# Optimization experiments

Hardware: AMD Instinct MI355X
Metric: run time of the kernel (lower is better)

Reference implementation:

```python
import jax, jax.numpy as jnp
import numpy as np

N_SRC = 50000   # nodes of src type
N_TRG = 50000   # nodes of trg type
H = 256         # hidden_size
E = 300000      # number of labeled edges for this message type


def setup_inputs() -> dict:
    key = jax.random.key(0)
    k0, k1, k2, k3 = jax.random.split(key, 4)
    x_src = jax.random.normal(k0, (N_SRC, H), dtype=jnp.float32)
    x_trg = jax.random.normal(k1, (N_TRG, H), dtype=jnp.float32)
    # nn.Parameter(torch.rand(H, H) * 0.01)
    R = jax.random.uniform(k2, (H, H), dtype=jnp.float32) * 0.01
    edge_index = jax.random.randint(k3, (2, E), 0, N_SRC, dtype=jnp.int64)
    return {"x_src": x_src, "x_trg": x_trg, "R": R, "edge_index": edge_index}


def reference(x_src, x_trg, R, edge_index):
    # Gather per-edge endpoint embeddings (index_select on dim 0).
    nodes_left = x_src[edge_index[0]]    # (E, H)
    nodes_right = x_trg[edge_index[1]]   # (E, H)
    # Original: sum((nodes_right @ R) @ nodes_left.T, dim=-1)
    # == (nodes_right @ R) @ nodes_left.sum(0)  -- same math, avoids the E x E
    # intermediate which is infeasible to materialize at this scale.
    left_sum = nodes_left.sum(axis=0)    # (H,)
    scores = (nodes_right @ R) @ left_sum  # (E,)
    return scores
```

## Files before the change

### kernel.cpp

```cpp
#include <hip/hip_runtime.h>

#define HDIM 256
#define CSB  1024
#define RDB  1024

__global__ void k_zero(uint4* __restrict__ p, int n4) {
    int i = blockIdx.x * blockDim.x + threadIdx.x;
    if (i < n4) p[i] = make_uint4(0u, 0u, 0u, 0u);
}

__global__ void k_count(const int4* __restrict__ src4, const int* __restrict__ src,
                        int E, unsigned int* __restrict__ cnt) {
    int i = blockIdx.x * blockDim.x + threadIdx.x;
    int E4 = E >> 2;
    if (i < E4) {
        int4 v = src4[i];
        atomicAdd(&cnt[v.x], 1u); atomicAdd(&cnt[v.y], 1u);
        atomicAdd(&cnt[v.z], 1u); atomicAdd(&cnt[v.w], 1u);
    }
    if (i < (E & 3)) atomicAdd(&cnt[src[(E4 << 2) + i]], 1u);
}

__global__ __launch_bounds__(256)
void k_colsum(const float4* __restrict__ xs4, const unsigned int* __restrict__ cnt,
              int Ns, float* __restrict__ pT) {
    const int lane = threadIdx.x & 63;
    const int wv = blockIdx.x * 4 + (threadIdx.x >> 6);
    const int NW = CSB * 4;
    float4 acc = make_float4(0.f, 0.f, 0.f, 0.f);

    float c0 = 0.f, c1 = 0.f, c2 = 0.f, c3 = 0.f;
    float4 x0 = make_float4(0,0,0,0), x1 = x0, x2 = x0, x3 = x0;
    int r = wv;
    if (r          < Ns) { c0 = (float)cnt[r];          x0 = xs4[(size_t)r * 64 + lane]; }
    if (r + NW     < Ns) { c1 = (float)cnt[r + NW];     x1 = xs4[(size_t)(r + NW) * 64 + lane]; }
    if (r + 2 * NW < Ns) { c2 = (float)cnt[r + 2 * NW]; x2 = xs4[(size_t)(r + 2 * NW) * 64 + lane]; }
    if (r + 3 * NW < Ns) { c3 = (float)cnt[r + 3 * NW]; x3 = xs4[(size_t)(r + 3 * NW) * 64 + lane]; }

    for (; r + 7 * NW < Ns; r += 4 * NW) {
        const int p = r + 4 * NW;
        float  nc0 = (float)cnt[p];           float4 nx0 = xs4[(size_t)p * 64 + lane];
        float  nc1 = (float)cnt[p + NW];      float4 nx1 = xs4[(size_t)(p + NW) * 64 + lane];
        float  nc2 = (float)cnt[p + 2 * NW];  float4 nx2 = xs4[(size_t)(p + 2 * NW) * 64 + lane];
        float  nc3 = (float)cnt[p + 3 * NW];  float4 nx3 = xs4[(size_t)(p + 3 * NW) * 64 + lane];
        acc.x += c0 * x0.x; acc.y += c0 * x0.y; acc.z += c0 * x0.z; acc.w += c0 * x0.w;
        acc.x += c1 * x1.x; acc.y += c1 * x1.y; acc.z += c1 * x1.z; acc.w += c1 * x1.w;
        acc.x += c2 * x2.x; acc.y += c2 * x2.y; acc.z += c2 * x2.z; acc.w += c2 * x2.w;
        acc.x += c3 * x3.x; acc.y += c3 * x3.y; acc.z += c3 * x3.z; acc.w += c3 * x3.w;
        c0 = nc0; x0 = nx0; c1 = nc1; x1 = nx1;
        c2 = nc2; x2 = nx2; c3 = nc3; x3 = nx3;
    }
    acc.x += c0 * x0.x; acc.y += c0 * x0.y; acc.z += c0 * x0.z; acc.w += c0 * x0.w;
    acc.x += c1 * x1.x; acc.y += c1 * x1.y; acc.z += c1 * x1.z; acc.w += c1 * x1.w;
    acc.x += c2 * x2.x; acc.y += c2 * x2.y; acc.z += c2 * x2.z; acc.w += c2 * x2.w;
    acc.x += c3 * x3.x; acc.y += c3 * x3.y; acc.z += c3 * x3.z; acc.w += c3 * x3.w;
    for (int s = r + 4 * NW; s < Ns; s += NW) {
        float  cc = (float)cnt[s];
        float4 xx = xs4[(size_t)s * 64 + lane];
        acc.x += cc * xx.x; acc.y += cc * xx.y; acc.z += cc * xx.z; acc.w += cc * xx.w;
    }

    __shared__ float s[4 * HDIM];
    const int col = lane * 4;
    const int rowOff = threadIdx.x >> 6;
    s[rowOff * HDIM + col + 0] = acc.x;
    s[rowOff * HDIM + col + 1] = acc.y;
    s[rowOff * HDIM + col + 2] = acc.z;
    s[rowOff * HDIM + col + 3] = acc.w;
    __syncthreads();
    const int tid = threadIdx.x;
    float part = (s[tid] + s[HDIM + tid]) + (s[2 * HDIM + tid] + s[3 * HDIM + tid]);
    pT[(size_t)tid * CSB + blockIdx.x] = part;
}

__global__ __launch_bounds__(256)
void k_reduceT(const float* __restrict__ pT, float* __restrict__ ls) {
    const int h = blockIdx.x;
    const int tid = threadIdx.x;
    const float* row = pT + (size_t)h * CSB;
    float a = (row[tid] + row[tid + 256]) + (row[tid + 512] + row[tid + 768]);
    #pragma unroll
    for (int o = 32; o > 0; o >>= 1) a += __shfl_down(a, o, 64);
    __shared__ float s[4];
    if ((tid & 63) == 0) s[tid >> 6] = a;
    __syncthreads();
    if (tid == 0) ls[h] = (s[0] + s[1]) + (s[2] + s[3]);
}

__global__ __launch_bounds__(256)
void k_matvec(const float* __restrict__ Rm, const float* __restrict__ ls,
              float* __restrict__ v) {
    const int i = blockIdx.x;
    const int tid = threadIdx.x;
    float a = Rm[(size_t)i * HDIM + tid] * ls[tid];
    #pragma unroll
    for (int o = 32; o > 0; o >>= 1) a += __shfl_down(a, o, 64);
    __shared__ float s[4];
    if ((tid & 63) == 0) s[tid >> 6] = a;
    __syncthreads();
    if (tid == 0) v[i] = (s[0] + s[1]) + (s[2] + s[3]);
}

__global__ __launch_bounds__(256)
void k_rowdot(const float4* __restrict__ xt4, const float* __restrict__ v,
              int N, float* __restrict__ t) {
    const int lane = threadIdx.x & 63;
    const float4 vr = ((const float4*)v)[lane];
    const int wv = blockIdx.x * 4 + (threadIdx.x >> 6);
    const int NW = RDB * 4;

    float4 x0 = make_float4(0,0,0,0), x1 = x0, x2 = x0, x3 = x0;
    int r = wv;
    if (r          < N) x0 = xt4[(size_t)r * 64 + lane];
    if (r + NW     < N) x1 = xt4[(size_t)(r + NW) * 64 + lane];
    if (r + 2 * NW < N) x2 = xt4[(size_t)(r + 2 * NW) * 64 + lane];
    if (r + 3 * NW < N) x3 = xt4[(size_t)(r + 3 * NW) * 64 + lane];

#define RD_DOT(X) ((X).x * vr.x + (X).y * vr.y + (X).z * vr.z + (X).w * vr.w)
    for (; r + 7 * NW < N; r += 4 * NW) {
        const int p = r + 4 * NW;
        float4 nx0 = xt4[(size_t)p * 64 + lane];
        float4 nx1 = xt4[(size_t)(p + NW) * 64 + lane];
        float4 nx2 = xt4[(size_t)(p + 2 * NW) * 64 + lane];
        float4 nx3 = xt4[(size_t)(p + 3 * NW) * 64 + lane];
        float d0 = RD_DOT(x0), d1 = RD_DOT(x1), d2 = RD_DOT(x2), d3 = RD_DOT(x3);
        #pragma unroll
        for (int o = 32; o > 0; o >>= 1) {
            d0 += __shfl_down(d0, o, 64); d1 += __shfl_down(d1, o, 64);
            d2 += __shfl_down(d2, o, 64); d3 += __shfl_down(d3, o, 64);
        }
        if (lane == 0) { t[r] = d0; t[r + NW] = d1; t[r + 2 * NW] = d2; t[r + 3 * NW] = d3; }
        x0 = nx0; x1 = nx1; x2 = nx2; x3 = nx3;
    }
    {
        float d0 = RD_DOT(x0), d1 = RD_DOT(x1), d2 = RD_DOT(x2), d3 = RD_DOT(x3);
        #pragma unroll
        for (int o = 32; o > 0; o >>= 1) {
            d0 += __shfl_down(d0, o, 64); d1 += __shfl_down(d1, o, 64);
            d2 += __shfl_down(d2, o, 64); d3 += __shfl_down(d3, o, 64);
        }
        if (lane == 0) {
            if (r          < N) t[r]          = d0;
            if (r + NW     < N) t[r + NW]     = d1;
            if (r + 2 * NW < N) t[r + 2 * NW] = d2;
            if (r + 3 * NW < N) t[r + 3 * NW] = d3;
        }
    }
    for (int s = r + 4 * NW; s < N; s += NW) {
        float4 xx = xt4[(size_t)s * 64 + lane];
        float d = RD_DOT(xx);
        #pragma unroll
        for (int o = 32; o > 0; o >>= 1) d += __shfl_down(d, o, 64);
        if (lane == 0) t[s] = d;
    }
#undef RD_DOT
}

__global__ void k_gather(const int4* __restrict__ trg4, const int* __restrict__ trg, int E,
                         const float* __restrict__ t,
                         float4* __restrict__ out4, float* __restrict__ out) {
    int i = blockIdx.x * blockDim.x + threadIdx.x;
    int E4 = E >> 2;
    if (i < E4) {
        int4 v = trg4[i];
        out4[i] = make_float4(t[v.x], t[v.y], t[v.z], t[v.w]);
    }
    if (i < (E & 3)) {
        int e = (E4 << 2) + i;
        out[e] = t[trg[e]];
    }
}

extern "C" void kernel_launch(void* const* d_in, const int* in_sizes, int n_in,
                              void* d_out, int out_size, void* d_ws, size_t ws_size,
                              hipStream_t stream) {
    const float* x_src = (const float*)d_in[0];
    const float* x_trg = (const float*)d_in[1];
    const float* Rm    = (const float*)d_in[2];
    const int*   edge  = (const int*)d_in[3];
    float* out = (float*)d_out;

    const int Ns = in_sizes[0] / HDIM;
    const int Nt = in_sizes[1] / HDIM;
    const int E  = in_sizes[3] / 2;

    char* ws = (char*)d_ws;
    size_t off = 0;
    auto alloc = [&](size_t bytes) -> void* {
        void* p = ws + off;
        off = (off + bytes + 255) & ~(size_t)255;
        return p;
    };
    unsigned int* cnt = (unsigned int*)alloc((size_t)Ns * sizeof(unsigned int));
    float* pT = (float*)alloc((size_t)HDIM * CSB * sizeof(float));
    float* ls = (float*)alloc(HDIM * sizeof(float));
    float* v  = (float*)alloc(HDIM * sizeof(float));
    float* t  = (float*)alloc((size_t)Nt * sizeof(float));
    (void)ws_size; (void)n_in; (void)out_size;

    const int n4 = (Ns + 3) / 4;
    k_zero<<<(n4 + 255) / 256, 256, 0, stream>>>((uint4*)cnt, n4);

    const int E4 = E >> 2;
    const int cntThreads = (E4 > 0 ? E4 : 1);
    k_count<<<(cntThreads + 255) / 256, 256, 0, stream>>>(
        (const int4*)edge, edge, E, cnt);

    k_colsum<<<CSB, 256, 0, stream>>>((const float4*)x_src, cnt, Ns, pT);

    k_reduceT<<<HDIM, 256, 0, stream>>>(pT, ls);

    k_matvec<<<HDIM, 256, 0, stream>>>(Rm, ls, v);

    k_rowdot<<<RDB, 256, 0, stream>>>((const float4*)x_trg, v, Nt, t);

    k_gather<<<(cntThreads + 255) / 256, 256, 0, stream>>>(
        (const int4*)(edge + E), edge + E, E, t, (float4*)out, out);
}
```

Baseline: 54.18 us.

## Fuse column-sum reduction into matvec and use 1024-thread colsum blocks

The column-sum kernel now runs 256 blocks of 1024 threads, reducing 16 wave partials in shared memory and writing row-major partials. The separate transpose-reduce and matvec kernels are merged into one kernel where each block redundantly sums the 256 partials before its dot product with a row of R. This removes one kernel launch and the transposed partial layout. In exchange, every matvec block re-reads the full 256x256 partial array, and the colsum runs fewer, larger blocks.

```diff
diff --git a/kernel.cpp b/kernel.cpp
--- a/kernel.cpp
+++ b/kernel.cpp
@@ -1,8 +1,10 @@
 #include <hip/hip_runtime.h>
 
 #define HDIM 256
-#define CSB  1024
+#define CSB  256
+#define CSW  (CSB * 16)
 #define RDB  1024
+#define RNW  (RDB * 4)
 
 __global__ void k_zero(uint4* __restrict__ p, int n4) {
     int i = blockIdx.x * blockDim.x + threadIdx.x;
@@ -21,12 +23,13 @@
     if (i < (E & 3)) atomicAdd(&cnt[src[(E4 << 2) + i]], 1u);
 }
 
-__global__ __launch_bounds__(256)
+__global__ __launch_bounds__(1024)
 void k_colsum(const float4* __restrict__ xs4, const unsigned int* __restrict__ cnt,
-              int Ns, float* __restrict__ pT) {
+              int Ns, float* __restrict__ P) {
     const int lane = threadIdx.x & 63;
-    const int wv = blockIdx.x * 4 + (threadIdx.x >> 6);
-    const int NW = CSB * 4;
+    const int w    = threadIdx.x >> 6;
+    const int wv   = blockIdx.x * 16 + w;
+    const int NW   = CSW;
     float4 acc = make_float4(0.f, 0.f, 0.f, 0.f);
 
     float c0 = 0.f, c1 = 0.f, c2 = 0.f, c3 = 0.f;
@@ -60,45 +63,47 @@
         acc.x += cc * xx.x; acc.y += cc * xx.y; acc.z += cc * xx.z; acc.w += cc * xx.w;
     }
 
-    __shared__ float s[4 * HDIM];
+    __shared__ float s[16 * HDIM];
     const int col = lane * 4;
-    const int rowOff = threadIdx.x >> 6;
-    s[rowOff * HDIM + col + 0] = acc.x;
-    s[rowOff * HDIM + col + 1] = acc.y;
-    s[rowOff * HDIM + col + 2] = acc.z;
-    s[rowOff * HDIM + col + 3] = acc.w;
-    __syncthreads();
+    s[w * HDIM + col + 0] = acc.x;
+    s[w * HDIM + col + 1] = acc.y;
+    s[w * HDIM + col + 2] = acc.z;
+    s[w * HDIM + col + 3] = acc.w;
+    __syncthreads();
+    {
+        const int q = threadIdx.x >> 8;
+        const int h = threadIdx.x & 255;
+        float f = (s[(q * 4 + 0) * HDIM + h] + s[(q * 4 + 1) * HDIM + h])
+                + (s[(q * 4 + 2) * HDIM + h] + s[(q * 4 + 3) * HDIM + h]);
+        __syncthreads();
+        s[(q * 4) * HDIM + h] = f;
+    }
+    __syncthreads();
+    if (threadIdx.x < HDIM) {
+        const int h = threadIdx.x;
+        P[(size_t)blockIdx.x * HDIM + h] =
+            (s[0 * HDIM + h] + s[4 * HDIM + h]) + (s[8 * HDIM + h] + s[12 * HDIM + h]);
+    }
+}
+
+__global__ __launch_bounds__(256)
+void k_mv(const float* __restrict__ P, const float* __restrict__ Rm,
+          float* __restrict__ v) {
     const int tid = threadIdx.x;
-    float part = (s[tid] + s[HDIM + tid]) + (s[2 * HDIM + tid] + s[3 * HDIM + tid]);
-    pT[(size_t)tid * CSB + blockIdx.x] = part;
-}
-
-__global__ __launch_bounds__(256)
-void k_reduceT(const float* __restrict__ pT, float* __restrict__ ls) {
-    const int h = blockIdx.x;
-    const int tid = threadIdx.x;
-    const float* row = pT + (size_t)h * CSB;
-    float a = (row[tid] + row[tid + 256]) + (row[tid + 512] + row[tid + 768]);
+    __shared__ float lss[HDIM];
+    float a = 0.f;
+    #pragma unroll 16
+    for (int b = 0; b < CSB; ++b) a += P[(size_t)b * HDIM + tid];
+    lss[tid] = a;
+    __syncthreads();
+
+    float m = Rm[(size_t)blockIdx.x * HDIM + tid] * lss[tid];
     #pragma unroll
-    for (int o = 32; o > 0; o >>= 1) a += __shfl_down(a, o, 64);
+    for (int o = 32; o > 0; o >>= 1) m += __shfl_down(m, o, 64);
     __shared__ float s[4];
-    if ((tid & 63) == 0) s[tid >> 6] = a;
-    __syncthreads();
-    if (tid == 0) ls[h] = (s[0] + s[1]) + (s[2] + s[3]);
-}
-
-__global__ __launch_bounds__(256)
-void k_matvec(const float* __restrict__ Rm, const float* __restrict__ ls,
-              float* __restrict__ v) {
-    const int i = blockIdx.x;
-    const int tid = threadIdx.x;
-    float a = Rm[(size_t)i * HDIM + tid] * ls[tid];
-    #pragma unroll
-    for (int o = 32; o > 0; o >>= 1) a += __shfl_down(a, o, 64);
-    __shared__ float s[4];
-    if ((tid & 63) == 0) s[tid >> 6] = a;
-    __syncthreads();
-    if (tid == 0) v[i] = (s[0] + s[1]) + (s[2] + s[3]);
+    if ((tid & 63) == 0) s[tid >> 6] = m;
+    __syncthreads();
+    if (tid == 0) v[blockIdx.x] = (s[0] + s[1]) + (s[2] + s[3]);
 }
 
 __global__ __launch_bounds__(256)
@@ -107,7 +112,7 @@
     const int lane = threadIdx.x & 63;
     const float4 vr = ((const float4*)v)[lane];
     const int wv = blockIdx.x * 4 + (threadIdx.x >> 6);
-    const int NW = RDB * 4;
+    const int NW = RNW;
 
     float4 x0 = make_float4(0,0,0,0), x1 = x0, x2 = x0, x3 = x0;
     int r = wv;
@@ -192,8 +197,7 @@
         return p;
     };
     unsigned int* cnt = (unsigned int*)alloc((size_t)Ns * sizeof(unsigned int));
-    float* pT = (float*)alloc((size_t)HDIM * CSB * sizeof(float));
-    float* ls = (float*)alloc(HDIM * sizeof(float));
+    float* P  = (float*)alloc((size_t)CSB * HDIM * sizeof(float));
     float* v  = (float*)alloc(HDIM * sizeof(float));
     float* t  = (float*)alloc((size_t)Nt * sizeof(float));
     (void)ws_size; (void)n_in; (void)out_size;
@@ -206,11 +210,9 @@
     k_count<<<(cntThreads + 255) / 256, 256, 0, stream>>>(
         (const int4*)edge, edge, E, cnt);
 
-    k_colsum<<<CSB, 256, 0, stream>>>((const float4*)x_src, cnt, Ns, pT);
-
-    k_reduceT<<<HDIM, 256, 0, stream>>>(pT, ls);
-
-    k_matvec<<<HDIM, 256, 0, stream>>>(Rm, ls, v);
+    k_colsum<<<CSB, 1024, 0, stream>>>((const float4*)x_src, cnt, Ns, P);
+
+    k_mv<<<HDIM, 256, 0, stream>>>(P, Rm, v);
 
     k_rowdot<<<RDB, 256, 0, stream>>>((const float4*)x_trg, v, Nt, t);
 
```

Result: slower. 55.41 us (+2.3%).
